# Kernel tuning notes

Measured on AMD Instinct MI355X. Metric: run time of the kernel, lower is better.

## Reference

```python
import jax, jax.numpy as jnp
import numpy as np

B, T, K, H = 8192, 96, 32, 768  # batch, max_len, output_dim (tags), bert hidden


def setup_inputs() -> dict:
    key = jax.random.key(0)
    k1, k2, k3, k4 = jax.random.split(key, 4)
    hidden = jax.random.normal(k1, (B, H), dtype=jnp.float32)
    target = jax.random.randint(k2, (B, T), 0, K, dtype=jnp.int32)
    # Dense(output_dim * max_len) params
    W = jax.random.normal(k3, (H, T * K), dtype=jnp.float32) * 0.02
    b = jnp.zeros((T * K,), dtype=jnp.float32)
    # tf.random.uniform transition matrix
    transitions = jax.random.uniform(k4, (K, K), dtype=jnp.float32)
    return {"hidden": hidden, "target": target, "W": W, "b": b, "transitions": transitions}


def _crf_log_norm(em_tm, transitions):
    # em_tm: [T, B, K] time-major emissions. Forward algorithm (logsumexp recurrence).
    def step(alpha, em_t):
        # alpha: [B, K]; broadcast over next-tag axis
        new = jax.nn.logsumexp(alpha[:, :, None] + transitions[None, :, :], axis=1) + em_t
        return new, None
    alpha, _ = jax.lax.scan(step, em_tm[0], em_tm[1:])
    return jax.nn.logsumexp(alpha, axis=-1)  # [B]


def _crf_sequence_score(em_btk, target, transitions):
    # unary: emission score at gold tags; binary: transition scores along gold path
    unary = jnp.take_along_axis(em_btk, target[..., None], axis=-1)[..., 0].sum(-1)
    binary = transitions[target[:, :-1], target[:, 1:]].sum(-1)
    return unary + binary  # [B]


def _viterbi_decode(em_tm, transitions):
    # em_tm: [T, B, K]. Max-product forward pass collecting backpointers.
    def fwd(v, em_t):
        scores = v[:, :, None] + transitions[None, :, :]  # [B, K_prev, K_next]
        bp = jnp.argmax(scores, axis=1).astype(jnp.int32)  # [B, K]
        return jnp.max(scores, axis=1) + em_t, bp
    v, bps = jax.lax.scan(fwd, em_tm[0], em_tm[1:])  # bps: [T-1, B, K]
    last_tag = jnp.argmax(v, axis=-1).astype(jnp.int32)  # [B]
    # backtrace (reverse scan); output index i is the tag at time i
    def back(tag, bp_t):
        prev = jnp.take_along_axis(bp_t, tag[:, None], axis=1)[:, 0]
        return prev, prev
    _, prevs = jax.lax.scan(back, last_tag, bps, reverse=True)  # [T-1, B]
    tags = jnp.concatenate([prevs, last_tag[None, :]], axis=0)  # [T, B]
    return jnp.transpose(tags), jnp.max(v, axis=-1)


def reference(hidden, target, W, b, transitions):
    # Dense with sigmoid, then reshape to (B, max_len, output_dim)
    em = jax.nn.sigmoid(hidden @ W + b).reshape(hidden.shape[0], T, K)
    em_tm = jnp.transpose(em, (1, 0, 2))  # time-major for scan
    log_likelihood = _crf_sequence_score(em, target, transitions) - _crf_log_norm(em_tm, transitions)
    decode_predict, _ = _viterbi_decode(em_tm, transitions)
    return decode_predict, log_likelihood
```

## Files before the change

### kernel.cpp

```cpp
#include <hip/hip_runtime.h>
#include <cstdint>
#include <cstddef>

#define B_  8192
#define T_  96
#define K_  32
#define H_  768
#define NK_ (T_ * K_)

typedef __attribute__((ext_vector_type(8))) _Float16 f16x8;
typedef __attribute__((ext_vector_type(4))) float    f32x4;
typedef __attribute__((ext_vector_type(2))) float    f32x2;

#define SCALE_UP   4096.0f
#define SCALE_DOWN (1.0f / 16777216.0f)

__device__ __forceinline__ void load_lds16(const void* g, void* l) {
    __builtin_amdgcn_global_load_lds(
        (const __attribute__((address_space(1))) unsigned int*)g,
        (__attribute__((address_space(3))) unsigned int*)l,
        16, 0, 0);
}

__device__ __forceinline__ f32x2 pk_add(f32x2 a, f32x2 b) {
    f32x2 d;
    asm("v_pk_add_f32 %0, %1, %2" : "=v"(d) : "v"(a), "v"(b));
    return d;
}
__device__ __forceinline__ f32x2 pk_fma(f32x2 a, f32x2 b, f32x2 c) {
    f32x2 d;
    asm("v_pk_fma_f32 %0, %1, %2, %3" : "=v"(d) : "v"(a), "v"(b), "v"(c));
    return d;
}

__global__ __launch_bounds__(256) void splitA_kernel(
    const float* __restrict__ A, _Float16* __restrict__ Ath, _Float16* __restrict__ Atl)
{
    const int g   = blockIdx.x * 256 + threadIdx.x;
    const int row = g / 96;
    const int o   = g - row * 96;
    const int ks  = o >> 2, qq = o & 3;
    const int r   = row & 127, rb = row >> 7;
    const size_t dst = (size_t)(rb * 24 + ks) * 4096 + r * 32 + ((qq ^ ((r >> 1) & 3)) << 3);

    f32x4 v0 = *(const f32x4*)(A + (size_t)row * H_ + o * 8);
    f32x4 v1 = *(const f32x4*)(A + (size_t)row * H_ + o * 8 + 4);
    f16x8 hi, lo;
#pragma unroll
    for (int e = 0; e < 8; e++) {
        float x = ((e < 4) ? v0[e] : v1[e - 4]) * SCALE_UP;
        _Float16 h = (_Float16)x;
        hi[e] = h;
        lo[e] = (_Float16)(x - (float)h);
    }
    *(f16x8*)&Ath[dst] = hi;
    *(f16x8*)&Atl[dst] = lo;
}

__global__ __launch_bounds__(256) void splitW_kernel(
    const float* __restrict__ W, _Float16* __restrict__ Wth, _Float16* __restrict__ Wtl)
{
    const int g   = blockIdx.x * 256 + threadIdx.x;
    const int ko  = g / NK_;
    const int col = g - ko * NK_;
    const int k0  = ko * 8;
    const int cb  = col >> 7, n = col & 127;
    const int ks  = k0 >> 5, qq = (k0 & 31) >> 3;
    const size_t dst = (size_t)(cb * 24 + ks) * 4096 + n * 32 + ((qq ^ ((n >> 1) & 3)) << 3);

    f16x8 hi, lo;
#pragma unroll
    for (int j = 0; j < 8; j++) {
        float x = W[(size_t)(k0 + j) * NK_ + col] * SCALE_UP;
        _Float16 h = (_Float16)x;
        hi[j] = h;
        lo[j] = (_Float16)(x - (float)h);
    }
    *(f16x8*)&Wth[dst] = hi;
    *(f16x8*)&Wtl[dst] = lo;
}

__global__ __launch_bounds__(256, 2) void gemm_mfma_sigmoid_kernel(
    const _Float16* __restrict__ Ath, const _Float16* __restrict__ Atl,
    const _Float16* __restrict__ Wth, const _Float16* __restrict__ Wtl,
    const float* __restrict__ bias, float* __restrict__ em)
{
    __shared__ _Float16 lds[2][4][4096];

    const int tid  = threadIdx.x;
    const int cb   = blockIdx.x;
    const int rb   = blockIdx.y;
    const int lane = tid & 63;
    const int w    = tid >> 6;
    const int wr   = w >> 1, wc = w & 1;
    const int fr   = lane & 15;
    const int kg   = lane >> 4;

    const _Float16* srcs[4] = {
        Ath + (size_t)(rb * 24) * 4096, Atl + (size_t)(rb * 24) * 4096,
        Wth + (size_t)(cb * 24) * 4096, Wtl + (size_t)(cb * 24) * 4096 };

    auto stage = [&](int ks, int bb) {
#pragma unroll
        for (int m = 0; m < 4; m++) {
            const _Float16* s = srcs[m] + (size_t)ks * 4096 + w * 1024 + lane * 8;
            _Float16* d = &lds[bb][m][w * 1024];
            load_lds16(s, d);
            load_lds16(s + 512, d + 512);
        }
    };

    f32x4 acc[4][4];
#pragma unroll
    for (int i = 0; i < 4; i++)
#pragma unroll
        for (int j = 0; j < 4; j++) acc[i][j] = (f32x4)0.0f;

    int cur = 0;
    stage(0, 0);

    for (int ks = 0; ks < 24; ks++) {
        __syncthreads();
        if (ks + 1 < 24) stage(ks + 1, cur ^ 1);

        f16x8 fah[4], fal[4], fbh[4], fbl[4];
#pragma unroll
        for (int mi = 0; mi < 4; mi++) {
            const int r   = wr * 64 + mi * 16 + fr;
            const int idx = r * 32 + ((kg ^ ((r >> 1) & 3)) << 3);
            fah[mi] = *(const f16x8*)&lds[cur][0][idx];
            fal[mi] = *(const f16x8*)&lds[cur][1][idx];
        }
#pragma unroll
        for (int ni = 0; ni < 4; ni++) {
            const int r   = wc * 64 + ni * 16 + fr;
            const int idx = r * 32 + ((kg ^ ((r >> 1) & 3)) << 3);
            fbh[ni] = *(const f16x8*)&lds[cur][2][idx];
            fbl[ni] = *(const f16x8*)&lds[cur][3][idx];
        }
#pragma unroll
        for (int mi = 0; mi < 4; mi++)
#pragma unroll
            for (int ni = 0; ni < 4; ni++) {
                acc[mi][ni] = __builtin_amdgcn_mfma_f32_16x16x32_f16(fah[mi], fbh[ni], acc[mi][ni], 0, 0, 0);
                acc[mi][ni] = __builtin_amdgcn_mfma_f32_16x16x32_f16(fah[mi], fbl[ni], acc[mi][ni], 0, 0, 0);
                acc[mi][ni] = __builtin_amdgcn_mfma_f32_16x16x32_f16(fal[mi], fbh[ni], acc[mi][ni], 0, 0, 0);
            }
        cur ^= 1;
    }

    const int er = rb * 128 + wr * 64 + (lane >> 4) * 4;
    const int ec = cb * 128 + wc * 64 + fr;
#pragma unroll
    for (int ni = 0; ni < 4; ni++) {
        const int   gc = ec + ni * 16;
        const float bv = bias[gc];
#pragma unroll
        for (int mi = 0; mi < 4; mi++)
#pragma unroll
            for (int r = 0; r < 4; r++) {
                const int gr = er + mi * 16 + r;
                float x = acc[mi][ni][r] * SCALE_DOWN + bv;
                em[(size_t)gr * NK_ + gc] = 1.0f / (1.0f + __expf(-x));
            }
    }
}

__global__ __launch_bounds__(256) void crf_scan16_kernel(
    const float* __restrict__ em,
    const int* __restrict__ target,
    const float* __restrict__ trans,
    float* __restrict__ out_tags,
    float* __restrict__ ll)
{
    __shared__ float trans_s[K_ * K_];
    __shared__ float es[16][40];
    __shared__ float vs[16][40];
    __shared__ unsigned int bp_s[16][24][K_];
    __shared__ unsigned char tgt_s[16][T_];

    const int tid = threadIdx.x;
    const int g   = tid >> 4;
    const int l   = tid & 15;
    const int b   = blockIdx.x * 16 + g;

    for (int i = tid; i < K_ * K_; i += 256) trans_s[i] = trans[i];
    __syncthreads();

    f32x2 t2a[16], t2b[16], E2a[16], E2b[16];
#pragma unroll
    for (int c = 0; c < 16; c++) {
        float a0 = trans_s[(2 * c) * K_ + l];
        float a1 = trans_s[(2 * c + 1) * K_ + l];
        float b0 = trans_s[(2 * c) * K_ + l + 16];
        float b1 = trans_s[(2 * c + 1) * K_ + l + 16];
        t2a[c] = (f32x2){a0, a1};  E2a[c] = (f32x2){__expf(a0), __expf(a1)};
        t2b[c] = (f32x2){b0, b1};  E2b[c] = (f32x2){__expf(b0), __expf(b1)};
    }

    const float* emb = em + (size_t)b * NK_;

    int tg[6];
#pragma unroll
    for (int j = 0; j < 6; j++) {
        tg[j] = target[b * T_ + l + 16 * j];
        tgt_s[g][l + 16 * j] = (unsigned char)tg[j];
    }
    __builtin_amdgcn_wave_barrier();
    float gold = 0.0f;
#pragma unroll
    for (int j = 0; j < 6; j++) {
        const int t = l + 16 * j;
        gold += emb[t * K_ + tg[j]];
        if (t > 0) gold += trans_s[(int)tgt_s[g][t - 1] * K_ + tg[j]];
    }

    const float em_a = emb[l];
    const float em_b = emb[l + 16];
    float Ea = __expf(em_a), Eb = __expf(em_b);
    float va = em_a,         vb = em_b;
    int   expo_sum = 0;
    unsigned int bpwa = 0, bpwb = 0;

    float na = emb[K_ + l];
    float nb = emb[K_ + l + 16];

    auto STEP = [&](int t, int sh) {
        const float cem_a = na, cem_b = nb;
        na = emb[(t + 1) * K_ + l];
        nb = emb[(t + 1) * K_ + l + 16];

        es[g][l] = Ea;  es[g][l + 16] = Eb;
        vs[g][l] = va;  vs[g][l + 16] = vb;
        __builtin_amdgcn_wave_barrier();

        f32x2 aa0 = (f32x2){0.0f, 0.0f}, aa1 = aa0, ab0 = aa0, ab1 = aa0;
        float bva = -1e30f, bvb = -1e30f;
        int   bia = 0, bib = 0;
#pragma unroll
        for (int j = 0; j < 8; j++) {
            f32x4 eq = *(const f32x4*)&es[g][4 * j];
            f32x4 vq = *(const f32x4*)&vs[g][4 * j];
            f32x2 e0 = (f32x2){eq[0], eq[1]};
            f32x2 e1 = (f32x2){eq[2], eq[3]};
            f32x2 v0 = (f32x2){vq[0], vq[1]};
            f32x2 v1 = (f32x2){vq[2], vq[3]};

            aa0 = pk_fma(e0, E2a[2 * j], aa0);
            aa1 = pk_fma(e1, E2a[2 * j + 1], aa1);
            ab0 = pk_fma(e0, E2b[2 * j], ab0);
            ab1 = pk_fma(e1, E2b[2 * j + 1], ab1);

            {
                f32x2 s0 = pk_add(v0, t2a[2 * j]);
                f32x2 s1 = pk_add(v1, t2a[2 * j + 1]);
                float w0 = (s0[1] > s0[0]) ? s0[1] : s0[0];
                int   i0 = (s0[1] > s0[0]) ? (4 * j + 1) : (4 * j);
                float w1 = (s1[1] > s1[0]) ? s1[1] : s1[0];
                int   i1 = (s1[1] > s1[0]) ? (4 * j + 3) : (4 * j + 2);
                if (w1 > w0) { w0 = w1; i0 = i1; }
                if (w0 > bva) { bva = w0; bia = i0; }
            }
            {
                f32x2 s0 = pk_add(v0, t2b[2 * j]);
                f32x2 s1 = pk_add(v1, t2b[2 * j + 1]);
                float w0 = (s0[1] > s0[0]) ? s0[1] : s0[0];
                int   i0 = (s0[1] > s0[0]) ? (4 * j + 1) : (4 * j);
                float w1 = (s1[1] > s1[0]) ? s1[1] : s1[0];
                int   i1 = (s1[1] > s1[0]) ? (4 * j + 3) : (4 * j + 2);
                if (w1 > w0) { w0 = w1; i0 = i1; }
                if (w0 > bvb) { bvb = w0; bib = i0; }
            }
        }
        f32x2 sa = pk_add(aa0, aa1);
        f32x2 sb = pk_add(ab0, ab1);
        Ea = (sa[0] + sa[1]) * __expf(cem_a - 4.0f);
        Eb = (sb[0] + sb[1]) * __expf(cem_b - 4.0f);
        va = bva + cem_a;
        vb = bvb + cem_b;

        bpwa |= (unsigned int)bia << (8 * sh);
        bpwb |= (unsigned int)bib << (8 * sh);
        if (sh == 3) {
            bp_s[g][(t - 1) >> 2][l]      = bpwa;
            bp_s[g][(t - 1) >> 2][l + 16] = bpwb;
            bpwa = 0; bpwb = 0;
        }
        __builtin_amdgcn_wave_barrier();
    };

    auto RENORM = [&]() {
        float m = fmaxf(Ea, Eb);
#pragma unroll
        for (int d = 8; d >= 1; d >>= 1) m = fmaxf(m, __shfl_xor(m, d));
        const unsigned int ebits = (__float_as_uint(m) >> 23) & 255u;
        const float s = __uint_as_float((254u - ebits) << 23);
        Ea *= s; Eb *= s;
        expo_sum += (int)ebits - 127;
    };

    for (int tb = 1; tb <= 89; tb += 4) {
        STEP(tb, 0); STEP(tb + 1, 1); STEP(tb + 2, 2); STEP(tb + 3, 3);
        if ((tb & 7) == 5) RENORM();
    }
    STEP(93, 0); STEP(94, 1); STEP(95, 2);
    bp_s[g][23][l]      = bpwa;
    bp_s[g][23][l + 16] = bpwb;
    __builtin_amdgcn_wave_barrier();

    float S = Ea + Eb;
#pragma unroll
    for (int d = 8; d >= 1; d >>= 1) S += __shfl_xor(S, d);
    const float logZ = __logf(S) + 380.0f + (float)expo_sum * 0.69314718055994531f;

    float gsum = gold;
#pragma unroll
    for (int d = 8; d >= 1; d >>= 1) gsum += __shfl_xor(gsum, d);

    float bv = va; int bi = l;
    if (vb > bv) { bv = vb; bi = l + 16; }
#pragma unroll
    for (int d = 8; d >= 1; d >>= 1) {
        float ov = __shfl_xor(bv, d);
        int   oi = __shfl_xor(bi, d);
        if (ov > bv || (ov == bv && oi < bi)) { bv = ov; bi = oi; }
    }

    if (l == 0) {
        ll[b] = gsum - logZ;
        float* ot = out_tags + (size_t)b * T_;
        int tag = bi;
        ot[T_ - 1] = (float)tag;
        for (int t = T_ - 2; t >= 0; t--) {
            unsigned int wd = bp_s[g][t >> 2][tag];
            tag = (wd >> (8 * (t & 3))) & 0xFF;
            ot[t] = (float)tag;
        }
    }
}

extern "C" void kernel_launch(void* const* d_in, const int* in_sizes, int n_in,
                              void* d_out, int out_size, void* d_ws, size_t ws_size,
                              hipStream_t stream)
{
    const float* hidden = (const float*)d_in[0];
    const int*   target = (const int*)d_in[1];
    const float* W      = (const float*)d_in[2];
    const float* bias   = (const float*)d_in[3];
    const float* trans  = (const float*)d_in[4];

    float* out      = (float*)d_out;
    float* out_tags = out;
    float* out_ll   = out + (size_t)B_ * T_;

    char* ws = (char*)d_ws;
    const size_t emB = (size_t)B_ * NK_ * 4;
    const size_t ahB = (size_t)B_ * H_ * 2;
    const size_t whB = (size_t)H_ * NK_ * 2;

    float*    em  = (float*)ws;
    _Float16* Ath = (_Float16*)(ws + emB);
    _Float16* Atl = (_Float16*)(ws + emB + ahB);
    _Float16* Wth = (_Float16*)(ws + emB + 2 * ahB);
    _Float16* Wtl = (_Float16*)(ws + emB + 2 * ahB + whB);

    splitA_kernel<<<(B_ * 96) / 256, 256, 0, stream>>>(hidden, Ath, Atl);
    splitW_kernel<<<(NK_ * 96) / 256, 256, 0, stream>>>(W, Wth, Wtl);

    dim3 gemm_grid(NK_ / 128, B_ / 128);
    gemm_mfma_sigmoid_kernel<<<gemm_grid, 256, 0, stream>>>(Ath, Atl, Wth, Wtl, bias, em);

    crf_scan16_kernel<<<B_ / 16, 256, 0, stream>>>(em, target, trans, out_tags, out_ll);
}
```

Baseline: 266.2 us.

## Split CRF forward and Viterbi passes into separate block roles

The CRF kernel now launches twice as many blocks, with even blocks running the logsumexp forward recurrence and odd blocks running the Viterbi max/argmax pass plus backtrace. Each role holds only its own transition registers, with scalar FMAs replacing the packed-f32 inline asm, and backpointers are packed as 5-bit fields, six per word. The aim is to shorten each block's serial dependency chain, cut register pressure so more waves fit per CU (launch bounds of 4), and shrink LDS use. In exchange, every emission row is read from global memory twice, and the two roles do different amounts of work per block, which can leave the load uneven.

```diff
diff --git a/kernel.cpp b/kernel.cpp
--- a/kernel.cpp
+++ b/kernel.cpp
@@ -10,7 +10,6 @@
 
 typedef __attribute__((ext_vector_type(8))) _Float16 f16x8;
 typedef __attribute__((ext_vector_type(4))) float    f32x4;
-typedef __attribute__((ext_vector_type(2))) float    f32x2;
 
 #define SCALE_UP   4096.0f
 #define SCALE_DOWN (1.0f / 16777216.0f)
@@ -20,17 +19,6 @@
         (const __attribute__((address_space(1))) unsigned int*)g,
         (__attribute__((address_space(3))) unsigned int*)l,
         16, 0, 0);
-}
-
-__device__ __forceinline__ f32x2 pk_add(f32x2 a, f32x2 b) {
-    f32x2 d;
-    asm("v_pk_add_f32 %0, %1, %2" : "=v"(d) : "v"(a), "v"(b));
-    return d;
-}
-__device__ __forceinline__ f32x2 pk_fma(f32x2 a, f32x2 b, f32x2 c) {
-    f32x2 d;
-    asm("v_pk_fma_f32 %0, %1, %2, %3" : "=v"(d) : "v"(a), "v"(b), "v"(c));
-    return d;
 }
 
 __global__ __launch_bounds__(256) void splitA_kernel(
@@ -166,175 +154,189 @@
     }
 }
 
-__global__ __launch_bounds__(256) void crf_scan16_kernel(
+__global__ __launch_bounds__(256, 4) void crf_fat_kernel(
     const float* __restrict__ em,
     const int* __restrict__ target,
     const float* __restrict__ trans,
     float* __restrict__ out_tags,
     float* __restrict__ ll)
 {
-    __shared__ float trans_s[K_ * K_];
-    __shared__ float es[16][40];
-    __shared__ float vs[16][40];
-    __shared__ unsigned int bp_s[16][24][K_];
-    __shared__ unsigned char tgt_s[16][T_];
-
-    const int tid = threadIdx.x;
-    const int g   = tid >> 4;
-    const int l   = tid & 15;
-    const int b   = blockIdx.x * 16 + g;
+    __shared__ __align__(16) char smem[4096 + 3072 + 32768];
+    float* trans_s = (float*)(smem);
+    float* exch    = (float*)(smem + 4096);
+
+    const int tid  = threadIdx.x;
+    const int role = blockIdx.x & 1;
+    const int bb   = blockIdx.x >> 1;
+    const int g    = tid >> 4;
+    const int l    = tid & 15;
+    const int b    = bb * 16 + g;
 
     for (int i = tid; i < K_ * K_; i += 256) trans_s[i] = trans[i];
     __syncthreads();
 
-    f32x2 t2a[16], t2b[16], E2a[16], E2b[16];
-#pragma unroll
-    for (int c = 0; c < 16; c++) {
-        float a0 = trans_s[(2 * c) * K_ + l];
-        float a1 = trans_s[(2 * c + 1) * K_ + l];
-        float b0 = trans_s[(2 * c) * K_ + l + 16];
-        float b1 = trans_s[(2 * c + 1) * K_ + l + 16];
-        t2a[c] = (f32x2){a0, a1};  E2a[c] = (f32x2){__expf(a0), __expf(a1)};
-        t2b[c] = (f32x2){b0, b1};  E2b[c] = (f32x2){__expf(b0), __expf(b1)};
-    }
-
     const float* emb = em + (size_t)b * NK_;
-
-    int tg[6];
-#pragma unroll
-    for (int j = 0; j < 6; j++) {
-        tg[j] = target[b * T_ + l + 16 * j];
-        tgt_s[g][l + 16 * j] = (unsigned char)tg[j];
-    }
-    __builtin_amdgcn_wave_barrier();
-    float gold = 0.0f;
-#pragma unroll
-    for (int j = 0; j < 6; j++) {
-        const int t = l + 16 * j;
-        gold += emb[t * K_ + tg[j]];
-        if (t > 0) gold += trans_s[(int)tgt_s[g][t - 1] * K_ + tg[j]];
-    }
-
-    const float em_a = emb[l];
-    const float em_b = emb[l + 16];
-    float Ea = __expf(em_a), Eb = __expf(em_b);
-    float va = em_a,         vb = em_b;
-    int   expo_sum = 0;
-    unsigned int bpwa = 0, bpwb = 0;
-
-    float na = emb[K_ + l];
-    float nb = emb[K_ + l + 16];
-
-    auto STEP = [&](int t, int sh) {
-        const float cem_a = na, cem_b = nb;
-        na = emb[(t + 1) * K_ + l];
-        nb = emb[(t + 1) * K_ + l + 16];
-
-        es[g][l] = Ea;  es[g][l + 16] = Eb;
-        vs[g][l] = va;  vs[g][l + 16] = vb;
+    float* ex = exch + g * 48;
+
+    if (role == 0) {
+        unsigned char* tgt_s = (unsigned char*)(smem + 7168) + g * T_;
+
+        float E2a[K_], E2b[K_];
+#pragma unroll
+        for (int p = 0; p < K_; p++) {
+            E2a[p] = __expf(trans_s[p * K_ + l]);
+            E2b[p] = __expf(trans_s[p * K_ + l + 16]);
+        }
+
+        int tg[6];
+#pragma unroll
+        for (int j = 0; j < 6; j++) {
+            tg[j] = target[b * T_ + l + 16 * j];
+            tgt_s[l + 16 * j] = (unsigned char)tg[j];
+        }
         __builtin_amdgcn_wave_barrier();
-
-        f32x2 aa0 = (f32x2){0.0f, 0.0f}, aa1 = aa0, ab0 = aa0, ab1 = aa0;
-        float bva = -1e30f, bvb = -1e30f;
-        int   bia = 0, bib = 0;
-#pragma unroll
-        for (int j = 0; j < 8; j++) {
-            f32x4 eq = *(const f32x4*)&es[g][4 * j];
-            f32x4 vq = *(const f32x4*)&vs[g][4 * j];
-            f32x2 e0 = (f32x2){eq[0], eq[1]};
-            f32x2 e1 = (f32x2){eq[2], eq[3]};
-            f32x2 v0 = (f32x2){vq[0], vq[1]};
-            f32x2 v1 = (f32x2){vq[2], vq[3]};
-
-            aa0 = pk_fma(e0, E2a[2 * j], aa0);
-            aa1 = pk_fma(e1, E2a[2 * j + 1], aa1);
-            ab0 = pk_fma(e0, E2b[2 * j], ab0);
-            ab1 = pk_fma(e1, E2b[2 * j + 1], ab1);
-
-            {
-                f32x2 s0 = pk_add(v0, t2a[2 * j]);
-                f32x2 s1 = pk_add(v1, t2a[2 * j + 1]);
-                float w0 = (s0[1] > s0[0]) ? s0[1] : s0[0];
-                int   i0 = (s0[1] > s0[0]) ? (4 * j + 1) : (4 * j);
-                float w1 = (s1[1] > s1[0]) ? s1[1] : s1[0];
-                int   i1 = (s1[1] > s1[0]) ? (4 * j + 3) : (4 * j + 2);
-                if (w1 > w0) { w0 = w1; i0 = i1; }
-                if (w0 > bva) { bva = w0; bia = i0; }
-            }
-            {
-                f32x2 s0 = pk_add(v0, t2b[2 * j]);
-                f32x2 s1 = pk_add(v1, t2b[2 * j + 1]);
-                float w0 = (s0[1] > s0[0]) ? s0[1] : s0[0];
-                int   i0 = (s0[1] > s0[0]) ? (4 * j + 1) : (4 * j);
-                float w1 = (s1[1] > s1[0]) ? s1[1] : s1[0];
-                int   i1 = (s1[1] > s1[0]) ? (4 * j + 3) : (4 * j + 2);
-                if (w1 > w0) { w0 = w1; i0 = i1; }
-                if (w0 > bvb) { bvb = w0; bib = i0; }
-            }
-        }
-        f32x2 sa = pk_add(aa0, aa1);
-        f32x2 sb = pk_add(ab0, ab1);
-        Ea = (sa[0] + sa[1]) * __expf(cem_a - 4.0f);
-        Eb = (sb[0] + sb[1]) * __expf(cem_b - 4.0f);
-        va = bva + cem_a;
-        vb = bvb + cem_b;
-
-        bpwa |= (unsigned int)bia << (8 * sh);
-        bpwb |= (unsigned int)bib << (8 * sh);
-        if (sh == 3) {
-            bp_s[g][(t - 1) >> 2][l]      = bpwa;
-            bp_s[g][(t - 1) >> 2][l + 16] = bpwb;
-            bpwa = 0; bpwb = 0;
-        }
+        float gold = 0.0f;
+#pragma unroll
+        for (int j = 0; j < 6; j++) {
+            const int t = l + 16 * j;
+            gold += emb[t * K_ + tg[j]];
+            if (t > 0) gold += trans_s[(int)tgt_s[t - 1] * K_ + tg[j]];
+        }
+
+        float Ea = __expf(emb[l]);
+        float Eb = __expf(emb[l + 16]);
+        int   expo_sum = 0;
+        float na = emb[K_ + l];
+        float nb = emb[K_ + l + 16];
+
+        auto STEPF = [&](int t) {
+            const float cem_a = na, cem_b = nb;
+            na = emb[(t + 1) * K_ + l];
+            nb = emb[(t + 1) * K_ + l + 16];
+            ex[l] = Ea;  ex[l + 16] = Eb;
+            __builtin_amdgcn_wave_barrier();
+            float sa = 0.0f, sb = 0.0f;
+#pragma unroll
+            for (int q = 0; q < 8; q++) {
+                f32x4 eq = *(const f32x4*)&ex[4 * q];
+#pragma unroll
+                for (int e = 0; e < 4; e++) {
+                    sa = fmaf(eq[e], E2a[4 * q + e], sa);
+                    sb = fmaf(eq[e], E2b[4 * q + e], sb);
+                }
+            }
+            Ea = sa * __expf(cem_a - 4.0f);
+            Eb = sb * __expf(cem_b - 4.0f);
+            __builtin_amdgcn_wave_barrier();
+        };
+
+        auto RENORM = [&]() {
+            float m = fmaxf(Ea, Eb);
+#pragma unroll
+            for (int d = 8; d >= 1; d >>= 1) m = fmaxf(m, __shfl_xor(m, d));
+            const unsigned int ebits = (__float_as_uint(m) >> 23) & 255u;
+            const float s = __uint_as_float((254u - ebits) << 23);
+            Ea *= s; Eb *= s;
+            expo_sum += (int)ebits - 127;
+        };
+
+        for (int tb = 1; tb <= 89; tb += 4) {
+            STEPF(tb); STEPF(tb + 1); STEPF(tb + 2); STEPF(tb + 3);
+            if ((tb & 7) == 5) RENORM();
+        }
+        STEPF(93); STEPF(94); STEPF(95);
+
+        float S = Ea + Eb;
+#pragma unroll
+        for (int d = 8; d >= 1; d >>= 1) S += __shfl_xor(S, d);
+        const float logZ = __logf(S) + 380.0f + (float)expo_sum * 0.69314718055994531f;
+
+        float gsum = gold;
+#pragma unroll
+        for (int d = 8; d >= 1; d >>= 1) gsum += __shfl_xor(gsum, d);
+
+        if (l == 0) ll[b] = gsum - logZ;
+
+    } else {
+        unsigned int* bp5 = (unsigned int*)(smem + 7168) + g * (K_ * 16);
+
+        float tca[K_], tcb[K_];
+#pragma unroll
+        for (int p = 0; p < K_; p++) {
+            tca[p] = trans_s[p * K_ + l];
+            tcb[p] = trans_s[p * K_ + l + 16];
+        }
+
+        float va = emb[l];
+        float vb = emb[l + 16];
+        unsigned int bpwa = 0, bpwb = 0;
+        float na = emb[K_ + l];
+        float nb = emb[K_ + l + 16];
+
+        auto STEPV = [&](int t, int sh) {
+            const float cem_a = na, cem_b = nb;
+            na = emb[(t + 1) * K_ + l];
+            nb = emb[(t + 1) * K_ + l + 16];
+            ex[l] = va;  ex[l + 16] = vb;
+            __builtin_amdgcn_wave_barrier();
+            float bva = -1e30f, bvb = -1e30f;
+            int   bia = 0, bib = 0;
+#pragma unroll
+            for (int q = 0; q < 8; q++) {
+                f32x4 vq = *(const f32x4*)&ex[4 * q];
+#pragma unroll
+                for (int e = 0; e < 4; e++) {
+                    const int p = 4 * q + e;
+                    float sa = vq[e] + tca[p];
+                    if (sa > bva) { bva = sa; bia = p; }
+                    float sb2 = vq[e] + tcb[p];
+                    if (sb2 > bvb) { bvb = sb2; bib = p; }
+                }
+            }
+            va = bva + cem_a;
+            vb = bvb + cem_b;
+            bpwa |= (unsigned int)bia << (5 * sh);
+            bpwb |= (unsigned int)bib << (5 * sh);
+            if (sh == 5) {
+                bp5[l * 16 + (t - 1) / 6]        = bpwa;
+                bp5[(l + 16) * 16 + (t - 1) / 6] = bpwb;
+                bpwa = 0; bpwb = 0;
+            }
+            __builtin_amdgcn_wave_barrier();
+        };
+
+        for (int tb = 1; tb <= 73; tb += 12) {
+            STEPV(tb + 0, 0); STEPV(tb + 1, 1); STEPV(tb + 2, 2);
+            STEPV(tb + 3, 3); STEPV(tb + 4, 4); STEPV(tb + 5, 5);
+            STEPV(tb + 6, 0); STEPV(tb + 7, 1); STEPV(tb + 8, 2);
+            STEPV(tb + 9, 3); STEPV(tb + 10, 4); STEPV(tb + 11, 5);
+        }
+        STEPV(85, 0); STEPV(86, 1); STEPV(87, 2);
+        STEPV(88, 3); STEPV(89, 4); STEPV(90, 5);
+        STEPV(91, 0); STEPV(92, 1); STEPV(93, 2);
+        STEPV(94, 3); STEPV(95, 4);
+        bp5[l * 16 + 15]        = bpwa;
+        bp5[(l + 16) * 16 + 15] = bpwb;
         __builtin_amdgcn_wave_barrier();
-    };
-
-    auto RENORM = [&]() {
-        float m = fmaxf(Ea, Eb);
-#pragma unroll
-        for (int d = 8; d >= 1; d >>= 1) m = fmaxf(m, __shfl_xor(m, d));
-        const unsigned int ebits = (__float_as_uint(m) >> 23) & 255u;
-        const float s = __uint_as_float((254u - ebits) << 23);
-        Ea *= s; Eb *= s;
-        expo_sum += (int)ebits - 127;
-    };
-
-    for (int tb = 1; tb <= 89; tb += 4) {
-        STEP(tb, 0); STEP(tb + 1, 1); STEP(tb + 2, 2); STEP(tb + 3, 3);
-        if ((tb & 7) == 5) RENORM();
-    }
-    STEP(93, 0); STEP(94, 1); STEP(95, 2);
-    bp_s[g][23][l]      = bpwa;
-    bp_s[g][23][l + 16] = bpwb;
-    __builtin_amdgcn_wave_barrier();
-
-    float S = Ea + Eb;
-#pragma unroll
-    for (int d = 8; d >= 1; d >>= 1) S += __shfl_xor(S, d);
-    const float logZ = __logf(S) + 380.0f + (float)expo_sum * 0.69314718055994531f;
-
-    float gsum = gold;
-#pragma unroll
-    for (int d = 8; d >= 1; d >>= 1) gsum += __shfl_xor(gsum, d);
-
-    float bv = va; int bi = l;
-    if (vb > bv) { bv = vb; bi = l + 16; }
-#pragma unroll
-    for (int d = 8; d >= 1; d >>= 1) {
-        float ov = __shfl_xor(bv, d);
-        int   oi = __shfl_xor(bi, d);
-        if (ov > bv || (ov == bv && oi < bi)) { bv = ov; bi = oi; }
-    }
-
-    if (l == 0) {
-        ll[b] = gsum - logZ;
-        float* ot = out_tags + (size_t)b * T_;
-        int tag = bi;
-        ot[T_ - 1] = (float)tag;
-        for (int t = T_ - 2; t >= 0; t--) {
-            unsigned int wd = bp_s[g][t >> 2][tag];
-            tag = (wd >> (8 * (t & 3))) & 0xFF;
-            ot[t] = (float)tag;
+
+        float bv = va; int bi = l;
+        if (vb > bv) { bv = vb; bi = l + 16; }
+#pragma unroll
+        for (int d = 8; d >= 1; d >>= 1) {
+            float ov = __shfl_xor(bv, d);
+            int   oi = __shfl_xor(bi, d);
+            if (ov > bv || (ov == bv && oi < bi)) { bv = ov; bi = oi; }
+        }
+
+        if (l == 0) {
+            float* ot = out_tags + (size_t)b * T_;
+            int tag = bi;
+            ot[T_ - 1] = (float)tag;
+            for (int t = T_ - 2; t >= 0; t--) {
+                unsigned int wd = bp5[tag * 16 + t / 6];
+                tag = (int)((wd >> (5 * (t % 6))) & 31u);
+                ot[t] = (float)tag;
+            }
         }
     }
 }
@@ -370,5 +372,5 @@
     dim3 gemm_grid(NK_ / 128, B_ / 128);
     gemm_mfma_sigmoid_kernel<<<gemm_grid, 256, 0, stream>>>(Ath, Atl, Wth, Wtl, bias, em);
 
-    crf_scan16_kernel<<<B_ / 16, 256, 0, stream>>>(em, target, trans, out_tags, out_ll);
-}
+    crf_fat_kernel<<<1024, 256, 0, stream>>>(em, target, trans, out_tags, out_ll);
+}
```

Measured after the change: 345.2 us. 1.3x slower.

## Remap GEMM workgroups for XCD locality and use compiler vector intrinsics in CRF

Applied to the files above, without the earlier changes.

The GEMM launch changes from a 2D grid to a 1D grid of 1536 blocks. Each block id is remapped so that consecutive blocks placed round-robin on the 8 XCDs cover contiguous (row, column) tiles, which should improve L2 reuse of A and W tiles within each XCD. Separately, the inline-asm packed FMA/add helpers in the CRF scan are replaced by elementwise builtins and plain vector ops. This lets the compiler schedule the operations itself, though it may not always emit packed instructions.

```diff
diff --git a/kernel.cpp b/kernel.cpp
--- a/kernel.cpp
+++ b/kernel.cpp
@@ -20,17 +20,6 @@
         (const __attribute__((address_space(1))) unsigned int*)g,
         (__attribute__((address_space(3))) unsigned int*)l,
         16, 0, 0);
-}
-
-__device__ __forceinline__ f32x2 pk_add(f32x2 a, f32x2 b) {
-    f32x2 d;
-    asm("v_pk_add_f32 %0, %1, %2" : "=v"(d) : "v"(a), "v"(b));
-    return d;
-}
-__device__ __forceinline__ f32x2 pk_fma(f32x2 a, f32x2 b, f32x2 c) {
-    f32x2 d;
-    asm("v_pk_fma_f32 %0, %1, %2, %3" : "=v"(d) : "v"(a), "v"(b), "v"(c));
-    return d;
 }
 
 __global__ __launch_bounds__(256) void splitA_kernel(
@@ -88,8 +77,10 @@
     __shared__ _Float16 lds[2][4][4096];
 
     const int tid  = threadIdx.x;
-    const int cb   = blockIdx.x;
-    const int rb   = blockIdx.y;
+    const int bid  = blockIdx.x;
+    const int wgid = (bid & 7) * 192 + (bid >> 3);
+    const int cb   = wgid % 24;
+    const int rb   = wgid / 24;
     const int lane = tid & 63;
     const int w    = tid >> 6;
     const int wr   = w >> 1, wc = w & 1;
@@ -246,14 +237,14 @@
             f32x2 v0 = (f32x2){vq[0], vq[1]};
             f32x2 v1 = (f32x2){vq[2], vq[3]};
 
-            aa0 = pk_fma(e0, E2a[2 * j], aa0);
-            aa1 = pk_fma(e1, E2a[2 * j + 1], aa1);
-            ab0 = pk_fma(e0, E2b[2 * j], ab0);
-            ab1 = pk_fma(e1, E2b[2 * j + 1], ab1);
+            aa0 = __builtin_elementwise_fma(e0, E2a[2 * j], aa0);
+            aa1 = __builtin_elementwise_fma(e1, E2a[2 * j + 1], aa1);
+            ab0 = __builtin_elementwise_fma(e0, E2b[2 * j], ab0);
+            ab1 = __builtin_elementwise_fma(e1, E2b[2 * j + 1], ab1);
 
             {
-                f32x2 s0 = pk_add(v0, t2a[2 * j]);
-                f32x2 s1 = pk_add(v1, t2a[2 * j + 1]);
+                f32x2 s0 = v0 + t2a[2 * j];
+                f32x2 s1 = v1 + t2a[2 * j + 1];
                 float w0 = (s0[1] > s0[0]) ? s0[1] : s0[0];
                 int   i0 = (s0[1] > s0[0]) ? (4 * j + 1) : (4 * j);
                 float w1 = (s1[1] > s1[0]) ? s1[1] : s1[0];
@@ -262,8 +253,8 @@
                 if (w0 > bva) { bva = w0; bia = i0; }
             }
             {
-                f32x2 s0 = pk_add(v0, t2b[2 * j]);
-                f32x2 s1 = pk_add(v1, t2b[2 * j + 1]);
+                f32x2 s0 = v0 + t2b[2 * j];
+                f32x2 s1 = v1 + t2b[2 * j + 1];
                 float w0 = (s0[1] > s0[0]) ? s0[1] : s0[0];
                 int   i0 = (s0[1] > s0[0]) ? (4 * j + 1) : (4 * j);
                 float w1 = (s1[1] > s1[0]) ? s1[1] : s1[0];
@@ -272,8 +263,8 @@
                 if (w0 > bvb) { bvb = w0; bib = i0; }
             }
         }
-        f32x2 sa = pk_add(aa0, aa1);
-        f32x2 sb = pk_add(ab0, ab1);
+        f32x2 sa = aa0 + aa1;
+        f32x2 sb = ab0 + ab1;
         Ea = (sa[0] + sa[1]) * __expf(cem_a - 4.0f);
         Eb = (sb[0] + sb[1]) * __expf(cem_b - 4.0f);
         va = bva + cem_a;
@@ -367,8 +358,7 @@
     splitA_kernel<<<(B_ * 96) / 256, 256, 0, stream>>>(hidden, Ath, Atl);
     splitW_kernel<<<(NK_ * 96) / 256, 256, 0, stream>>>(W, Wth, Wtl);
 
-    dim3 gemm_grid(NK_ / 128, B_ / 128);
-    gemm_mfma_sigmoid_kernel<<<gemm_grid, 256, 0, stream>>>(Ath, Atl, Wth, Wtl, bias, em);
+    gemm_mfma_sigmoid_kernel<<<1536, 256, 0, stream>>>(Ath, Atl, Wth, Wtl, bias, em);
 
     crf_scan16_kernel<<<B_ / 16, 256, 0, stream>>>(em, target, trans, out_tags, out_ll);
 }
```

New measurement: 266.5 us. About the same (+0.1%).
